# Optimization experiments

Measured on AMD Instinct MI355X. Metric: run time of the kernel, lower is better.

The kernel has to match this reference:

```python
import jax, jax.numpy as jnp
import numpy as np

K = 16  # neighbors per point (init kwarg k)


def setup_inputs() -> dict:
    key = jax.random.key(0)
    k0, k1, k2 = jax.random.split(key, 3)
    B, N, C, L, O = 4, 8192, 32, 64, 128
    return {
        "x": jax.random.normal(k0, (B, N, C), dtype=jnp.float32),
        "W_lin": jax.random.normal(k1, (C, L), dtype=jnp.float32) * 0.1,
        "b_lin": jnp.zeros((L,), dtype=jnp.float32),
        "W_conv": jax.random.normal(k2, (L, O), dtype=jnp.float32) * 0.1,
        "b_conv": jnp.zeros((O,), dtype=jnp.float32),
    }


def reference(x, W_lin, b_lin, W_conv, b_conv):
    # --- knn(x, k): squared-euclidean pairwise distance + top-k nearest ---
    sq = jnp.sum(x * x, axis=-1)                                   # [B,N]
    # dist[b,i,j] = ||x_i - x_j||^2  (self included, dist 0)
    dist = sq[:, :, None] - 2.0 * jnp.einsum('bnc,bmc->bnm', x, x) + sq[:, None, :]
    _, idx = jax.lax.top_k(-dist, K)                               # [B,N,K] int32
    # --- index_points: gather neighbor features ---
    knn_x = jax.vmap(lambda xb, ib: xb[ib])(x, idx)                # [B,N,K,C]
    # --- max pool over neighbors ---
    pooled = jnp.max(knn_x, axis=2)                                # [B,N,C]
    # --- Dense(linear) -> Conv1D(out_channel, kernel_size=1) -> relu ---
    h = pooled @ W_lin + b_lin                                     # [B,N,64]
    h = h @ W_conv + b_conv                                        # [B,N,128]
    return jax.nn.relu(h)
```

## Files before the change

kernel.cpp:

```cpp
#include <hip/hip_runtime.h>

#define NPTS   8192
#define CCH    32
#define LDIM   64
#define ODIM   128
#define KNN    16
#define QPB    64
#define TILEC  64
#define NTIL   128
#define TREC   4352
#define NBLK   ((4 * NPTS) / QPB)
#define SCAP   57
#define MARGIN 0.75f

typedef _Float16 half8   __attribute__((ext_vector_type(8)));
typedef float    float4v __attribute__((ext_vector_type(4)));

#define OFF_SK   14592
#define OFF_T32  14592
#define OFF_SCN  29184
#define OFF_TQ   29440
#define OFF_KN   29696
#define OFF_HH   8448
#define LDS_BYTES 33792

__global__ void prep_kernel(const float* __restrict__ x, float* __restrict__ sqg,
                            char* __restrict__ xh2) {
    int p = blockIdx.x * 256 + threadIdx.x;
    const float4* src = (const float4*)(x + (size_t)p * CCH);
    float4 f[8];
    #pragma unroll
    for (int k = 0; k < 8; ++k) f[k] = src[k];
    float s = 0.f;
    #pragma unroll
    for (int k = 0; k < 8; ++k)
        s += f[k].x * f[k].x + f[k].y * f[k].y + f[k].z * f[k].z + f[k].w * f[k].w;
    sqg[p] = s;
    int b = p >> 13, pp = p & (NPTS - 1);
    char* rec = xh2 + (size_t)b * NTIL * TREC + (size_t)(pp >> 6) * TREC;
    int st = (pp >> 4) & 3, col = pp & 15;
    char* fd = rec + st * 1024 + col * 16;
    #pragma unroll
    for (int q = 0; q < 4; ++q) {
        float4 a = f[2 * q], c = f[2 * q + 1];
        half8 h;
        h[0] = (_Float16)a.x; h[1] = (_Float16)a.y; h[2] = (_Float16)a.z; h[3] = (_Float16)a.w;
        h[4] = (_Float16)c.x; h[5] = (_Float16)c.y; h[6] = (_Float16)c.z; h[7] = (_Float16)c.w;
        *(half8*)(fd + q * 256) = h;
    }
    *(float*)(rec + 4096 + col * 16 + st * 4) = s;
}

__global__ __launch_bounds__(256, 2)
void graph_layer_kernel(const float* __restrict__ x,
                        const float* __restrict__ sqg,
                        const char* __restrict__ xh2,
                        const float* __restrict__ Wl,
                        const float* __restrict__ bl,
                        const float* __restrict__ Wc,
                        const float* __restrict__ bc,
                        float* __restrict__ out)
{
    __shared__ __align__(16) char smem[LDS_BYTES];
    int*   slist = (int*)smem;
    float* skeys = (float*)(smem + OFF_SK);
    float* t32   = (float*)(smem + OFF_T32);
    int*   scnt  = (int*)(smem + OFF_SCN);
    float* tq    = (float*)(smem + OFF_TQ);
    int*   kn    = (int*)(smem + OFF_KN);
    float* pl    = (float*)smem;
    float* hh    = (float*)(smem + OFF_HH);

    const int tid  = threadIdx.x;
    const int lane = tid & 63;
    const int w    = tid >> 6;
    const int col  = lane & 15;
    const int quad = lane >> 4;
    const float INF = __builtin_inff();

    const int qb0 = blockIdx.x * QPB;
    const int b   = qb0 >> 13;
    const int qbl = qb0 & (NPTS - 1);
    const int S   = blockIdx.x & (NTIL - 1);
    const float* xb  = x   + (size_t)(b << 13) * CCH;
    const float* sqb = sqg + (b << 13);
    const char*  xhb = xh2 + (size_t)b * NTIL * TREC;

    half8 qh;
    {
        int pp = qbl + w * 16 + col;
        qh = *(const half8*)(xhb + (size_t)(pp >> 6) * TREC
                             + ((pp >> 4) & 3) * 1024 + quad * 256 + col * 16);
        #pragma unroll
        for (int i = 0; i < 8; ++i) qh[i] = qh[i] * (_Float16)-2.0f;
    }

    const char* lbase = xhb + (size_t)lane * 16;
    const char* sbase = xhb + 4096 + (size_t)col * 16;

    half8 f0[4], f1[4], f2[4], f3[4];
    float4v s0v, s1v, s2v, s3v;

#define LDSET(F, SV, T) { \
        int _t = ((T) + S) & (NTIL - 1); \
        const char* _r = lbase + (size_t)_t * TREC; \
        F[0] = *(const half8*)(_r); \
        F[1] = *(const half8*)(_r + 1024); \
        F[2] = *(const half8*)(_r + 2048); \
        F[3] = *(const half8*)(_r + 3072); \
        SV = *(const float4v*)(sbase + (size_t)_t * TREC); \
    }

    float m1[4] = {INF, INF, INF, INF};
    float m2[4] = {INF, INF, INF, INF};

#define PASS1(F, SV) { \
        _Pragma("unroll") \
        for (int st = 0; st < 4; ++st) { \
            float sc = SV[st]; \
            float4v acc = __builtin_amdgcn_mfma_f32_16x16x32_f16( \
                qh, F[st], (float4v){sc, sc, sc, sc}, 0, 0, 0); \
            _Pragma("unroll") \
            for (int j = 0; j < 4; ++j) { \
                float key = acc[j]; \
                float o1  = m1[j]; \
                m1[j] = fminf(key, o1); \
                m2[j] = __builtin_amdgcn_fmed3f(key, o1, m2[j]); \
            } \
        } \
    }

    LDSET(f0, s0v, 0) LDSET(f1, s1v, 1) LDSET(f2, s2v, 2) LDSET(f3, s3v, 3)
    #pragma unroll 1
    for (int T = 0; T < NTIL; T += 4) {
        PASS1(f0, s0v) LDSET(f0, s0v, T + 4)
        PASS1(f1, s1v) LDSET(f1, s1v, T + 5)
        PASS1(f2, s2v) LDSET(f2, s2v, T + 6)
        PASS1(f3, s3v) LDSET(f3, s3v, T + 7)
    }

    #pragma unroll
    for (int j = 0; j < 4; ++j) {
        int qq = w * 16 + quad * 4 + j;
        t32[qq * 33 + col * 2 + 0] = m1[j];
        t32[qq * 33 + col * 2 + 1] = m2[j];
    }
    __syncthreads();
    {
        int q = tid & 63, wt = tid >> 6;
        float v[8]; int r[8];
        #pragma unroll
        for (int u = 0; u < 8; ++u) { v[u] = t32[q * 33 + wt * 8 + u]; r[u] = 0; }
        #pragma unroll 8
        for (int jj = 0; jj < 32; ++jj) {
            float vj = t32[q * 33 + jj];
            #pragma unroll
            for (int u = 0; u < 8; ++u)
                r[u] += (int)(vj < v[u]) | ((int)(vj == v[u]) & (int)(jj < wt * 8 + u));
        }
        #pragma unroll
        for (int u = 0; u < 8; ++u)
            if (r[u] == KNN - 1) tq[q] = v[u];
        if (tid < QPB) scnt[tid] = 0;
    }
    __syncthreads();
    float T2[4];
    #pragma unroll
    for (int j = 0; j < 4; ++j) T2[j] = tq[w * 16 + quad * 4 + j] + MARGIN;

#define PASS2(F, SV, T) { \
        int _tb = (((T) + S) & (NTIL - 1)) * TILEC; \
        _Pragma("unroll") \
        for (int st = 0; st < 4; ++st) { \
            float sc = SV[st]; \
            float4v acc = __builtin_amdgcn_mfma_f32_16x16x32_f16( \
                qh, F[st], (float4v){sc, sc, sc, sc}, 0, 0, 0); \
            _Pragma("unroll") \
            for (int j = 0; j < 4; ++j) { \
                float key = acc[j]; \
                if (key < T2[j]) { \
                    int qq = w * 16 + quad * 4 + j; \
                    int slot = atomicAdd(&scnt[qq], 1); \
                    if (slot < SCAP) slist[qq * SCAP + slot] = _tb + st * 16 + col; \
                } \
            } \
        } \
    }

    LDSET(f0, s0v, 0) LDSET(f1, s1v, 1) LDSET(f2, s2v, 2) LDSET(f3, s3v, 3)
    #pragma unroll 1
    for (int T = 0; T < NTIL; T += 4) {
        PASS2(f0, s0v, T)     LDSET(f0, s0v, T + 4)
        PASS2(f1, s1v, T + 1) LDSET(f1, s1v, T + 5)
        PASS2(f2, s2v, T + 2) LDSET(f2, s2v, T + 6)
        PASS2(f3, s3v, T + 3) LDSET(f3, s3v, T + 7)
    }
    __syncthreads();

    {
        int qq = tid & 63, sb4 = tid >> 6;
        int n = scnt[qq]; if (n > SCAP) n = SCAP;
        const float4* xi4 = (const float4*)(xb + (size_t)(qbl + qq) * CCH);
        for (int s = sb4; s < n; s += 4) {
            int jdx = slist[qq * SCAP + s];
            const float4* xj = (const float4*)(xb + (size_t)jdx * CCH);
            float a0 = 0.f, a1 = 0.f, a2 = 0.f, a3 = 0.f;
            #pragma unroll 2
            for (int k = 0; k < 8; ++k) {
                float4 cv = xj[k], qv = xi4[k];
                a0 = fmaf(cv.x, qv.x, a0); a1 = fmaf(cv.y, qv.y, a1);
                a2 = fmaf(cv.z, qv.z, a2); a3 = fmaf(cv.w, qv.w, a3);
            }
            float dot = (a0 + a1) + (a2 + a3);
            skeys[qq * SCAP + s] = fmaf(-2.f, dot, sqb[jdx]);
        }
    }
    __syncthreads();
    {
        int q = tid & 63, wt = tid >> 6;
        int n = scnt[q]; if (n > SCAP) n = SCAP;
        for (int s = wt; s < n; s += 4) {
            float k = skeys[q * SCAP + s];
            int   i = slist[q * SCAP + s];
            int rank = 0;
            #pragma unroll 4
            for (int jj = 0; jj < n; ++jj) {
                float kj = skeys[q * SCAP + jj];
                int   ij = slist[q * SCAP + jj];
                rank += (int)(kj < k) | ((int)(kj == k) & (int)(ij < i));
            }
            if (rank < KNN) kn[q * KNN + rank] = i;
        }
    }
    __syncthreads();

    {
        int q = tid >> 2, part = tid & 3;
        float4 m0 = make_float4(-INF, -INF, -INF, -INF);
        float4 mm1 = m0;
        #pragma unroll 4
        for (int k = 0; k < KNN; ++k) {
            int j = kn[q * KNN + k];
            const float4* r = (const float4*)(xb + (size_t)j * CCH + part * 8);
            float4 v0 = r[0], v1 = r[1];
            m0.x = fmaxf(m0.x, v0.x); m0.y = fmaxf(m0.y, v0.y);
            m0.z = fmaxf(m0.z, v0.z); m0.w = fmaxf(m0.w, v0.w);
            mm1.x = fmaxf(mm1.x, v1.x); mm1.y = fmaxf(mm1.y, v1.y);
            mm1.z = fmaxf(mm1.z, v1.z); mm1.w = fmaxf(mm1.w, v1.w);
        }
        float* d = pl + q * 33 + part * 8;
        d[0] = m0.x; d[1] = m0.y; d[2] = m0.z; d[3] = m0.w;
        d[4] = mm1.x; d[5] = mm1.y; d[6] = mm1.z; d[7] = mm1.w;
    }
    __syncthreads();
    {
        int l = tid & 63, qg2 = tid >> 6;
        #pragma unroll 1
        for (int qq = qg2; qq < QPB; qq += 4) {
            float acc = bl[l];
            #pragma unroll 8
            for (int c = 0; c < CCH; ++c)
                acc = fmaf(pl[qq * 33 + c], Wl[c * LDIM + l], acc);
            hh[qq * 65 + l] = acc;
        }
    }
    __syncthreads();
    {
        int o = tid & 127, qh2 = tid >> 7;
        #pragma unroll 1
        for (int qq = qh2; qq < QPB; qq += 2) {
            float acc = bc[o];
            #pragma unroll 8
            for (int l = 0; l < LDIM; ++l)
                acc = fmaf(hh[qq * 65 + l], Wc[l * ODIM + o], acc);
            out[(size_t)(qb0 + qq) * ODIM + o] = fmaxf(acc, 0.f);
        }
    }
}

extern "C" void kernel_launch(void* const* d_in, const int* in_sizes, int n_in,
                              void* d_out, int out_size, void* d_ws, size_t ws_size,
                              hipStream_t stream) {
    const float* x  = (const float*)d_in[0];
    const float* Wl = (const float*)d_in[1];
    const float* bl = (const float*)d_in[2];
    const float* Wc = (const float*)d_in[3];
    const float* bc = (const float*)d_in[4];
    float* out = (float*)d_out;
    float* sqf = (float*)d_ws;
    char*  xh2 = (char*)d_ws + 131072;
    (void)in_sizes; (void)n_in; (void)out_size; (void)ws_size;

    hipLaunchKernelGGL(prep_kernel, dim3((4 * NPTS) / 256), dim3(256), 0, stream, x, sqf, xh2);
    hipLaunchKernelGGL(graph_layer_kernel, dim3(NBLK), dim3(256), 0, stream,
                       x, sqf, xh2, Wl, bl, Wc, bc, out);
}
```

Baseline: 283.6 us.

## Split KNN scan across candidate chunks and merge partial top-k in separate kernel

The fused kernel is split in two. A scan kernel runs 4x more blocks, each covering one quarter of the candidate tiles, and writes per-chunk top-16 keys and 16-bit indices to workspace. A finish kernel merges the 64 candidates per query by rank counting, then does max-pooling and the two dense layers on 32-query blocks. The aim is more parallelism and occupancy by shortening each block's serial tile loop, at the cost of an extra launch, global round-trips for the partial results, and per-chunk thresholds that are less tight.

After: 401.6 us. 1.42x slower.

```diff
diff --git a/kernel.cpp b/kernel.cpp
--- a/kernel.cpp
+++ b/kernel.cpp
@@ -6,23 +6,21 @@
 #define ODIM   128
 #define KNN    16
 #define QPB    64
-#define TILEC  64
-#define NTIL   128
+#define NCHK   4
+#define NTILB  128
+#define NTILC  32
 #define TREC   4352
-#define NBLK   ((4 * NPTS) / QPB)
-#define SCAP   57
+#define SCAPC  50
+#define SKSTR  51
 #define MARGIN 0.75f
 
 typedef _Float16 half8   __attribute__((ext_vector_type(8)));
 typedef float    float4v __attribute__((ext_vector_type(4)));
 
-#define OFF_SK   14592
-#define OFF_T32  14592
-#define OFF_SCN  29184
-#define OFF_TQ   29440
-#define OFF_KN   29696
-#define OFF_HH   8448
-#define LDS_BYTES 33792
+#define LDSA 19968
+#define A_SL 13056
+#define A_SC 19456
+#define A_TQ 19712
 
 __global__ void prep_kernel(const float* __restrict__ x, float* __restrict__ sqg,
                             char* __restrict__ xh2) {
@@ -37,7 +35,7 @@
         s += f[k].x * f[k].x + f[k].y * f[k].y + f[k].z * f[k].z + f[k].w * f[k].w;
     sqg[p] = s;
     int b = p >> 13, pp = p & (NPTS - 1);
-    char* rec = xh2 + (size_t)b * NTIL * TREC + (size_t)(pp >> 6) * TREC;
+    char* rec = xh2 + (size_t)b * NTILB * TREC + (size_t)(pp >> 6) * TREC;
     int st = (pp >> 4) & 3, col = pp & 15;
     char* fd = rec + st * 1024 + col * 16;
     #pragma unroll
@@ -52,24 +50,18 @@
 }
 
 __global__ __launch_bounds__(256, 2)
-void graph_layer_kernel(const float* __restrict__ x,
-                        const float* __restrict__ sqg,
-                        const char* __restrict__ xh2,
-                        const float* __restrict__ Wl,
-                        const float* __restrict__ bl,
-                        const float* __restrict__ Wc,
-                        const float* __restrict__ bc,
-                        float* __restrict__ out)
+void scan_kernel(const float* __restrict__ x,
+                 const float* __restrict__ sqg,
+                 const char* __restrict__ xh2,
+                 float* __restrict__ kbuf,
+                 unsigned short* __restrict__ ibuf)
 {
-    __shared__ __align__(16) char smem[LDS_BYTES];
-    int*   slist = (int*)smem;
-    float* skeys = (float*)(smem + OFF_SK);
-    float* t32   = (float*)(smem + OFF_T32);
-    int*   scnt  = (int*)(smem + OFF_SCN);
-    float* tq    = (float*)(smem + OFF_TQ);
-    int*   kn    = (int*)(smem + OFF_KN);
-    float* pl    = (float*)smem;
-    float* hh    = (float*)(smem + OFF_HH);
+    __shared__ __align__(16) char smem[LDSA];
+    float*          t32   = (float*)smem;
+    float*          skeys = (float*)smem;
+    unsigned short* slist = (unsigned short*)(smem + A_SL);
+    int*            scnt  = (int*)(smem + A_SC);
+    float*          tq    = (float*)(smem + A_TQ);
 
     const int tid  = threadIdx.x;
     const int lane = tid & 63;
@@ -78,31 +70,34 @@
     const int quad = lane >> 4;
     const float INF = __builtin_inff();
 
-    const int qb0 = blockIdx.x * QPB;
-    const int b   = qb0 >> 13;
-    const int qbl = qb0 & (NPTS - 1);
-    const int S   = blockIdx.x & (NTIL - 1);
+    const int chunk = blockIdx.x >> 9;
+    const int qgi   = blockIdx.x & 511;
+    const int qb0   = qgi * QPB;
+    const int b     = qb0 >> 13;
+    const int qbl   = qb0 & (NPTS - 1);
+    const int S     = qgi & (NTILC - 1);
     const float* xb  = x   + (size_t)(b << 13) * CCH;
     const float* sqb = sqg + (b << 13);
-    const char*  xhb = xh2 + (size_t)b * NTIL * TREC;
+    const char*  xhb = xh2 + (size_t)b * NTILB * TREC;
+    const int ct0   = chunk * NTILC;
 
     half8 qh;
     {
         int pp = qbl + w * 16 + col;
         qh = *(const half8*)(xhb + (size_t)(pp >> 6) * TREC
-                             + ((pp >> 4) & 3) * 1024 + quad * 256 + col * 16);
+                             + ((pp >> 4) & 3) * 1024 + quad * 256 + (pp & 15) * 16);
         #pragma unroll
         for (int i = 0; i < 8; ++i) qh[i] = qh[i] * (_Float16)-2.0f;
     }
 
-    const char* lbase = xhb + (size_t)lane * 16;
-    const char* sbase = xhb + 4096 + (size_t)col * 16;
+    const char* lbase = xhb + (size_t)ct0 * TREC + (size_t)lane * 16;
+    const char* sbase = xhb + (size_t)ct0 * TREC + 4096 + (size_t)col * 16;
 
     half8 f0[4], f1[4], f2[4], f3[4];
     float4v s0v, s1v, s2v, s3v;
 
 #define LDSET(F, SV, T) { \
-        int _t = ((T) + S) & (NTIL - 1); \
+        int _t = ((T) + S) & (NTILC - 1); \
         const char* _r = lbase + (size_t)_t * TREC; \
         F[0] = *(const half8*)(_r); \
         F[1] = *(const half8*)(_r + 1024); \
@@ -132,7 +127,7 @@
 
     LDSET(f0, s0v, 0) LDSET(f1, s1v, 1) LDSET(f2, s2v, 2) LDSET(f3, s3v, 3)
     #pragma unroll 1
-    for (int T = 0; T < NTIL; T += 4) {
+    for (int T = 0; T < NTILC; T += 4) {
         PASS1(f0, s0v) LDSET(f0, s0v, T + 4)
         PASS1(f1, s1v) LDSET(f1, s1v, T + 5)
         PASS1(f2, s2v) LDSET(f2, s2v, T + 6)
@@ -169,7 +164,7 @@
     for (int j = 0; j < 4; ++j) T2[j] = tq[w * 16 + quad * 4 + j] + MARGIN;
 
 #define PASS2(F, SV, T) { \
-        int _tb = (((T) + S) & (NTIL - 1)) * TILEC; \
+        int _tb = (ct0 + (((T) + S) & (NTILC - 1))) * 64; \
         _Pragma("unroll") \
         for (int st = 0; st < 4; ++st) { \
             float sc = SV[st]; \
@@ -181,7 +176,9 @@
                 if (key < T2[j]) { \
                     int qq = w * 16 + quad * 4 + j; \
                     int slot = atomicAdd(&scnt[qq], 1); \
-                    if (slot < SCAP) slist[qq * SCAP + slot] = _tb + st * 16 + col; \
+                    if (slot < SCAPC) \
+                        slist[qq * SCAPC + slot] = \
+                            (unsigned short)(_tb + st * 16 + col); \
                 } \
             } \
         } \
@@ -189,7 +186,7 @@
 
     LDSET(f0, s0v, 0) LDSET(f1, s1v, 1) LDSET(f2, s2v, 2) LDSET(f3, s3v, 3)
     #pragma unroll 1
-    for (int T = 0; T < NTIL; T += 4) {
+    for (int T = 0; T < NTILC; T += 4) {
         PASS2(f0, s0v, T)     LDSET(f0, s0v, T + 4)
         PASS2(f1, s1v, T + 1) LDSET(f1, s1v, T + 5)
         PASS2(f2, s2v, T + 2) LDSET(f2, s2v, T + 6)
@@ -199,10 +196,10 @@
 
     {
         int qq = tid & 63, sb4 = tid >> 6;
-        int n = scnt[qq]; if (n > SCAP) n = SCAP;
+        int n = scnt[qq]; if (n > SCAPC) n = SCAPC;
         const float4* xi4 = (const float4*)(xb + (size_t)(qbl + qq) * CCH);
         for (int s = sb4; s < n; s += 4) {
-            int jdx = slist[qq * SCAP + s];
+            int jdx = slist[qq * SCAPC + s];
             const float4* xj = (const float4*)(xb + (size_t)jdx * CCH);
             float a0 = 0.f, a1 = 0.f, a2 = 0.f, a3 = 0.f;
             #pragma unroll 2
@@ -212,51 +209,100 @@
                 a2 = fmaf(cv.z, qv.z, a2); a3 = fmaf(cv.w, qv.w, a3);
             }
             float dot = (a0 + a1) + (a2 + a3);
-            skeys[qq * SCAP + s] = fmaf(-2.f, dot, sqb[jdx]);
+            skeys[qq * SKSTR + s] = fmaf(-2.f, dot, sqb[jdx]);
         }
     }
     __syncthreads();
     {
         int q = tid & 63, wt = tid >> 6;
-        int n = scnt[q]; if (n > SCAP) n = SCAP;
+        int n = scnt[q]; if (n > SCAPC) n = SCAPC;
+        float*          kdst = kbuf + (size_t)(qb0 + q) * 64 + chunk * KNN;
+        unsigned short* idst = ibuf + (size_t)(qb0 + q) * 64 + chunk * KNN;
         for (int s = wt; s < n; s += 4) {
-            float k = skeys[q * SCAP + s];
-            int   i = slist[q * SCAP + s];
+            float k = skeys[q * SKSTR + s];
+            int   i = slist[q * SCAPC + s];
             int rank = 0;
             #pragma unroll 4
             for (int jj = 0; jj < n; ++jj) {
-                float kj = skeys[q * SCAP + jj];
-                int   ij = slist[q * SCAP + jj];
+                float kj = skeys[q * SKSTR + jj];
+                int   ij = slist[q * SCAPC + jj];
+                rank += (int)(kj < k) | ((int)(kj == k) & (int)(ij < i));
+            }
+            if (rank < KNN) { kdst[rank] = k; idst[rank] = (unsigned short)i; }
+        }
+    }
+}
+
+#define LDSB 14976
+__global__ __launch_bounds__(256, 4)
+void finish_kernel(const float* __restrict__ x,
+                   const float* __restrict__ kbuf,
+                   const unsigned short* __restrict__ ibuf,
+                   const float* __restrict__ Wl,
+                   const float* __restrict__ bl,
+                   const float* __restrict__ Wc,
+                   const float* __restrict__ bc,
+                   float* __restrict__ out)
+{
+    __shared__ __align__(16) char smem[LDSB];
+    float*          mkeys = (float*)smem;
+    unsigned short* midx  = (unsigned short*)(smem + 8320);
+    int*            kn    = (int*)(smem + 12928);
+    float*          pl    = (float*)smem;
+    float*          hh    = (float*)(smem + 4224);
+
+    const int tid = threadIdx.x;
+    const int b   = blockIdx.x >> 8;
+    const int qbl = (blockIdx.x & 255) * 32;
+    const int qb0 = (b << 13) + qbl;
+    const float* xb = x + (size_t)(b << 13) * CCH;
+    const float INF = __builtin_inff();
+
+    {
+        int q = tid >> 3, c8 = (tid & 7) * 8;
+        const float4* ks = (const float4*)(kbuf + (size_t)(qb0 + q) * 64 + c8);
+        float4 k0 = ks[0], k1 = ks[1];
+        uint4 iv = *(const uint4*)(ibuf + (size_t)(qb0 + q) * 64 + c8);
+        float* kd = mkeys + q * 65 + c8;
+        kd[0] = k0.x; kd[1] = k0.y; kd[2] = k0.z; kd[3] = k0.w;
+        kd[4] = k1.x; kd[5] = k1.y; kd[6] = k1.z; kd[7] = k1.w;
+        *(uint4*)(midx + q * 72 + c8) = iv;
+    }
+    __syncthreads();
+    {
+        int q = tid >> 3, wt = tid & 7;
+        for (int c = wt; c < 64; c += 8) {
+            float k = mkeys[q * 65 + c];
+            int   i = midx[q * 72 + c];
+            int rank = 0;
+            #pragma unroll 4
+            for (int jj = 0; jj < 64; ++jj) {
+                float kj = mkeys[q * 65 + jj];
+                int   ij = midx[q * 72 + jj];
                 rank += (int)(kj < k) | ((int)(kj == k) & (int)(ij < i));
             }
             if (rank < KNN) kn[q * KNN + rank] = i;
         }
     }
     __syncthreads();
-
-    {
-        int q = tid >> 2, part = tid & 3;
+    {
+        int q = tid >> 3, part = tid & 7;
         float4 m0 = make_float4(-INF, -INF, -INF, -INF);
-        float4 mm1 = m0;
         #pragma unroll 4
         for (int k = 0; k < KNN; ++k) {
             int j = kn[q * KNN + k];
-            const float4* r = (const float4*)(xb + (size_t)j * CCH + part * 8);
-            float4 v0 = r[0], v1 = r[1];
-            m0.x = fmaxf(m0.x, v0.x); m0.y = fmaxf(m0.y, v0.y);
-            m0.z = fmaxf(m0.z, v0.z); m0.w = fmaxf(m0.w, v0.w);
-            mm1.x = fmaxf(mm1.x, v1.x); mm1.y = fmaxf(mm1.y, v1.y);
-            mm1.z = fmaxf(mm1.z, v1.z); mm1.w = fmaxf(mm1.w, v1.w);
-        }
-        float* d = pl + q * 33 + part * 8;
+            float4 v = *(const float4*)(xb + (size_t)j * CCH + part * 4);
+            m0.x = fmaxf(m0.x, v.x); m0.y = fmaxf(m0.y, v.y);
+            m0.z = fmaxf(m0.z, v.z); m0.w = fmaxf(m0.w, v.w);
+        }
+        float* d = pl + q * 33 + part * 4;
         d[0] = m0.x; d[1] = m0.y; d[2] = m0.z; d[3] = m0.w;
-        d[4] = mm1.x; d[5] = mm1.y; d[6] = mm1.z; d[7] = mm1.w;
     }
     __syncthreads();
     {
         int l = tid & 63, qg2 = tid >> 6;
         #pragma unroll 1
-        for (int qq = qg2; qq < QPB; qq += 4) {
+        for (int qq = qg2; qq < 32; qq += 4) {
             float acc = bl[l];
             #pragma unroll 8
             for (int c = 0; c < CCH; ++c)
@@ -268,7 +314,7 @@
     {
         int o = tid & 127, qh2 = tid >> 7;
         #pragma unroll 1
-        for (int qq = qh2; qq < QPB; qq += 2) {
+        for (int qq = qh2; qq < 32; qq += 2) {
             float acc = bc[o];
             #pragma unroll 8
             for (int l = 0; l < LDIM; ++l)
@@ -287,11 +333,16 @@
     const float* Wc = (const float*)d_in[3];
     const float* bc = (const float*)d_in[4];
     float* out = (float*)d_out;
-    float* sqf = (float*)d_ws;
-    char*  xh2 = (char*)d_ws + 131072;
+    float*          sqf  = (float*)d_ws;
+    char*           xh2  = (char*)d_ws + 131072;
+    float*          kbuf = (float*)((char*)d_ws + 2359296);
+    unsigned short* ibuf = (unsigned short*)((char*)d_ws + 10747904);
     (void)in_sizes; (void)n_in; (void)out_size; (void)ws_size;
 
-    hipLaunchKernelGGL(prep_kernel, dim3((4 * NPTS) / 256), dim3(256), 0, stream, x, sqf, xh2);
-    hipLaunchKernelGGL(graph_layer_kernel, dim3(NBLK), dim3(256), 0, stream,
-                       x, sqf, xh2, Wl, bl, Wc, bc, out);
+    hipLaunchKernelGGL(prep_kernel, dim3((4 * NPTS) / 256), dim3(256), 0, stream,
+                       x, sqf, xh2);
+    hipLaunchKernelGGL(scan_kernel, dim3(512 * NCHK), dim3(256), 0, stream,
+                       x, sqf, xh2, kbuf, ibuf);
+    hipLaunchKernelGGL(finish_kernel, dim3(1024), dim3(256), 0, stream,
+                       x, kbuf, ibuf, Wl, bl, Wc, bc, out);
 }
```
